# Kernel tuning notes

Hardware: AMD Instinct MI355X
Metric: run time of the kernel (lower is better)

Reference implementation:

```python
import jax, jax.numpy as jnp
import numpy as np

T, B, I, H, L = 512, 64, 512, 1024, 2

def setup_inputs() -> dict:
    key = jax.random.key(0)
    ks = jax.random.split(key, 9)
    stdv = 1.0 / np.sqrt(H)
    u = lambda k, shape: jax.random.uniform(k, shape, jnp.float32, -stdv, stdv)
    return {
        "x": jax.random.normal(ks[0], (T, B, I), jnp.float32),
        "w_ih0": u(ks[1], (4 * H, I)),
        "w_hh0": u(ks[2], (4 * H, H)),
        "b_ih0": u(ks[3], (4 * H,)),
        "b_hh0": u(ks[4], (4 * H,)),
        "w_ih1": u(ks[5], (4 * H, H)),
        "w_hh1": u(ks[6], (4 * H, H)),
        "b_ih1": u(ks[7], (4 * H,)),
        "b_hh1": u(ks[8], (4 * H,)),
    }

def _lstm_cell(x, h, c, w_ih, w_hh, b_ih, b_hh):
    # gates: [B, 4H]
    gates = x @ w_ih.T + b_ih + h @ w_hh.T + b_hh
    i, f, g, o = jnp.split(gates, 4, axis=1)
    c_new = jax.nn.sigmoid(f) * c + jax.nn.sigmoid(i) * jnp.tanh(g)
    h_new = jax.nn.sigmoid(o) * jnp.tanh(c_new)
    return h_new, c_new

def reference(x, w_ih0, w_hh0, b_ih0, b_hh0, w_ih1, w_hh1, b_ih1, b_hh1):
    layers = [(w_ih0, w_hh0, b_ih0, b_hh0), (w_ih1, w_hh1, b_ih1, b_hh1)]
    h0 = jnp.zeros((L, B, H), x.dtype)
    c0 = jnp.zeros((L, B, H), x.dtype)

    def step(carry, x_t):
        h, c = carry
        inp = x_t
        hs, cs = [], []
        for l, (w_ih, w_hh, b_ih, b_hh) in enumerate(layers):
            h_new, c_new = _lstm_cell(inp, h[l], c[l], w_ih, w_hh, b_ih, b_hh)
            hs.append(h_new)
            cs.append(c_new)
            inp = h_new
        return (jnp.stack(hs), jnp.stack(cs)), inp

    (h_f, c_f), out = jax.lax.scan(step, (h0, c0), x)
    return out, (h_f, c_f)
```

## Files before the change

kernel.cpp:

```cpp
#include <hip/hip_runtime.h>

#define TT 512
#define BB 64
#define II 512
#define HH 1024
#define NBLK 256
#define NTHR 512
#define FSTRIDE 32
#define SETSTRIDE (64 * FSTRIDE)

typedef short bf16x8 __attribute__((ext_vector_type(8)));
typedef float f32x4 __attribute__((ext_vector_type(4)));
typedef int   i32x4 __attribute__((ext_vector_type(4)));

struct Params {
  const unsigned short* xb;
  unsigned short* h0;
  unsigned short* h1;
  unsigned int* flags;
  const float* wih0; const float* whh0; const float* bih0; const float* bhh0;
  const float* wih1; const float* whh1; const float* bih1; const float* bhh1;
  float* out;
};

__device__ __forceinline__ unsigned short f2bf(float f) {
  unsigned int u = __float_as_uint(f);
  u += 0x7fffu + ((u >> 16) & 1u);
  return (unsigned short)(u >> 16);
}

__device__ __forceinline__ bf16x8 ld_bypass(const unsigned short* p) {
  i32x4 r;
  asm volatile("global_load_dwordx4 %0, %1, off sc0 sc1" : "=v"(r) : "v"(p));
  return __builtin_bit_cast(bf16x8, r);
}
__device__ __forceinline__ void st_bypass_b128(unsigned short* p, i32x4 v) {
  asm volatile("global_store_dwordx4 %0, %1, off sc0 sc1" :: "v"(p), "v"(v) : "memory");
}
__device__ __forceinline__ void st_bypass_u32(unsigned int* p, unsigned int v) {
  asm volatile("global_store_dword %0, %1, off sc0 sc1" :: "v"(p), "v"(v) : "memory");
}
__device__ __forceinline__ unsigned int ld_flag_bypass(const unsigned int* p) {
  unsigned int r;
  asm volatile("global_load_dword %0, %1, off sc0 sc1\n\t"
               "s_waitcnt vmcnt(0)" : "=v"(r) : "v"(p) : "memory");
  return r;
}

template <int SLP>
__device__ __forceinline__ void poll_set(const unsigned int* f, int lane,
                                         unsigned int tgt) {
  while (ld_flag_bypass(&f[lane * FSTRIDE]) < tgt)
    __builtin_amdgcn_s_sleep(SLP);
}

__global__ void cvt_kernel(const float* __restrict__ x, unsigned short* __restrict__ xb, int n8) {
  int i = blockIdx.x * blockDim.x + threadIdx.x;
  int stride = gridDim.x * blockDim.x;
  for (; i < n8; i += stride) {
    const float4* p = (const float4*)(x) + (size_t)i * 2;
    float4 a = p[0], b = p[1];
    bf16x8 v;
    v[0] = (short)f2bf(a.x); v[1] = (short)f2bf(a.y); v[2] = (short)f2bf(a.z); v[3] = (short)f2bf(a.w);
    v[4] = (short)f2bf(b.x); v[5] = (short)f2bf(b.y); v[6] = (short)f2bf(b.z); v[7] = (short)f2bf(b.w);
    ((bf16x8*)xb)[i] = v;
  }
}

template <int LAYER>
__device__ void body(const Params& P, float (*pbuf)[64][36], float (*cb)[16],
                     unsigned short (*hbuf)[16]) {
  constexpr int K   = (LAYER == 0) ? (II + HH) : (2 * HH);
  constexpr int KSL = K / (8 * 32);
  constexpr int NG  = KSL / 2;
  constexpr int KIH = (LAYER == 0) ? II : HH;

  const int tid  = threadIdx.x;
  const int lane = tid & 63;
  const int kh   = tid >> 6;
  const int lbid = blockIdx.x & 127;
  const int mh   = lbid >> 6;
  const int ns   = lbid & 63;
  const int l15  = lane & 15;
  const int lk8  = (lane >> 4) * 8;

  const int setL0 = mh;
  const int setL1 = 2 + mh;
  const int fset  = LAYER * 2 + mh;

  const float* wih = (LAYER == 0) ? P.wih0 : P.wih1;
  const float* whh = (LAYER == 0) ? P.whh0 : P.whh1;

  bf16x8 wf[4][KSL];
  #pragma unroll
  for (int nt = 0; nt < 4; ++nt) {
    const int row = nt * HH + ns * 16 + l15;
    #pragma unroll
    for (int ks = 0; ks < KSL; ++ks) {
      int k = kh * (KSL * 32) + ks * 32 + lk8;
      const float* src = (k < KIH) ? (wih + (size_t)row * KIH + k)
                                   : (whh + (size_t)row * HH + (k - KIH));
      const float4* p4 = (const float4*)src;
      float4 a = p4[0], b = p4[1];
      bf16x8 v;
      v[0] = (short)f2bf(a.x); v[1] = (short)f2bf(a.y); v[2] = (short)f2bf(a.z); v[3] = (short)f2bf(a.w);
      v[4] = (short)f2bf(b.x); v[5] = (short)f2bf(b.y); v[6] = (short)f2bf(b.z); v[7] = (short)f2bf(b.w);
      wf[nt][ks] = v;
    }
  }

  float bv[4];
  {
    const float* bi = (LAYER == 0) ? P.bih0 : P.bih1;
    const float* bh = (LAYER == 0) ? P.bhh0 : P.bhh1;
    int unit = ns * 16 + (tid & 15);
    #pragma unroll
    for (int g = 0; g < 4; ++g) bv[g] = bi[g * HH + unit] + bh[g * HH + unit];
  }

  if (tid < 128) {
    int q = tid >> 4, j = tid & 15;
    #pragma unroll
    for (int r = 0; r < 4; ++r) cb[q * 4 + r][j] = 0.f;
  }

  const size_t BH  = (size_t)BB * HH;
  const size_t TBH = (size_t)TT * BH;

  #pragma unroll 1
  for (int p = 0; p <= TT; ++p) {
    const int t = (LAYER == 0) ? p : p - 1;
    const bool active = (LAYER == 0) ? (p < TT) : (p >= 1);

    if (kh == 0 && p >= 1) {
      poll_set<1>(P.flags + (size_t)setL0 * SETSTRIDE, lane, (unsigned)p);
    }
    if (kh == 1) {
      if (LAYER == 0) {
        if (p >= 3) poll_set<8>(P.flags + (size_t)setL1 * SETSTRIDE, lane, (unsigned)(p - 2));
      } else {
        if (p >= 1) poll_set<1>(P.flags + (size_t)setL1 * SETSTRIDE, lane, (unsigned)p);
      }
    }
    __syncthreads();

    f32x4 acc[2][4];
    float hv[4];
    if (active) {
      #pragma unroll
      for (int mt = 0; mt < 2; ++mt)
        #pragma unroll
        for (int nt = 0; nt < 4; ++nt) acc[mt][nt] = f32x4{0.f, 0.f, 0.f, 0.f};

      const unsigned short* h0prev = P.h0 + (size_t)((t - 1) & 3) * BH;
      const unsigned short* h0cur  = P.h0 + (size_t)(t & 3) * BH;
      const unsigned short* h1prev = P.h1 + (size_t)((t - 1) & 3) * BH;

      bf16x8 af[2][2][2];

      auto issue_group = [&](int g, int pp) {
        #pragma unroll
        for (int ksb = 0; ksb < 2; ++ksb) {
          const int ks = g * 2 + ksb;
          const int k  = kh * (KSL * 32) + ks * 32 + lk8;
          #pragma unroll
          for (int mt = 0; mt < 2; ++mt) {
            const int m = mh * 32 + mt * 16 + l15;
            const unsigned short* src;
            if (LAYER == 0) {
              src = (k < II) ? (P.xb + ((size_t)t * BB + m) * II + k)
                             : (h0prev + (size_t)m * HH + (k - II));
            } else {
              src = (k < HH) ? (h0cur + (size_t)m * HH + k)
                             : (h1prev + (size_t)m * HH + (k - HH));
            }
            af[pp][ksb][mt] = ld_bypass(src);
          }
        }
      };

      issue_group(0, 0);
      issue_group(1, 1);
      #pragma unroll
      for (int g = 0; g < NG; ++g) {
        if (g < NG - 1) asm volatile("s_waitcnt vmcnt(4)" ::: "memory");
        else            asm volatile("s_waitcnt vmcnt(0)" ::: "memory");
        __builtin_amdgcn_sched_barrier(0);
        #pragma unroll
        for (int ksb = 0; ksb < 2; ++ksb) {
          const int ks = g * 2 + ksb;
          #pragma unroll
          for (int mt = 0; mt < 2; ++mt)
            #pragma unroll
            for (int nt = 0; nt < 4; ++nt)
              acc[mt][nt] = __builtin_amdgcn_mfma_f32_16x16x32_bf16(af[g & 1][ksb][mt], wf[nt][ks], acc[mt][nt], 0, 0, 0);
        }
        if (g + 2 < NG) issue_group(g + 2, g & 1);
      }

      if (kh >= 4) {
        #pragma unroll
        for (int mt = 0; mt < 2; ++mt)
          #pragma unroll
          for (int nt = 0; nt < 4; ++nt) {
            int col = nt * 16 + l15;
            int mb  = mt * 16 + (lane >> 4) * 4;
            *(f32x4*)&pbuf[kh - 4][col][mb] = acc[mt][nt];
          }
      }
    }
    __syncthreads();
    if (active && kh < 4) {
      #pragma unroll
      for (int mt = 0; mt < 2; ++mt)
        #pragma unroll
        for (int nt = 0; nt < 4; ++nt) {
          int col = nt * 16 + l15;
          int mb  = mt * 16 + (lane >> 4) * 4;
          f32x4 v = *(const f32x4*)&pbuf[kh][col][mb];
          acc[mt][nt] += v;
          *(f32x4*)&pbuf[kh][col][mb] = acc[mt][nt];
        }
    }
    __syncthreads();
    if (active && tid < 128) {
      int q = tid >> 4, j = tid & 15;
      f32x4 gv[4];
      #pragma unroll
      for (int g = 0; g < 4; ++g) {
        int col = g * 16 + j;
        f32x4 s = *(const f32x4*)&pbuf[0][col][q * 4];
        #pragma unroll
        for (int w = 1; w < 4; ++w) s += *(const f32x4*)&pbuf[w][col][q * 4];
        gv[g] = s;
      }
      #pragma unroll
      for (int r = 0; r < 4; ++r) {
        int m = q * 4 + r;
        float iv = 1.f / (1.f + __expf(-(gv[0][r] + bv[0])));
        float fv = 1.f / (1.f + __expf(-(gv[1][r] + bv[1])));
        float gg = tanhf(gv[2][r] + bv[2]);
        float ov = 1.f / (1.f + __expf(-(gv[3][r] + bv[3])));
        float c = fv * cb[m][j] + iv * gg;
        cb[m][j] = c;
        float h = ov * tanhf(c);
        hv[r] = h;
        hbuf[m][j] = f2bf(h);
      }
    }
    __syncthreads();
    if (tid < 64) {
      if (active) {
        int row  = tid >> 1;
        int half = tid & 1;
        i32x4 v = *(const i32x4*)&hbuf[row][half * 8];
        unsigned short* dst = ((LAYER == 0) ? P.h0 : P.h1) +
            (size_t)(t & 3) * BH + (size_t)(mh * 32 + row) * HH + ns * 16 + half * 8;
        st_bypass_b128(dst, v);
      }
      asm volatile("s_waitcnt vmcnt(0)" ::: "memory");
      if (tid == 0)
        st_bypass_u32(P.flags + (size_t)fset * SETSTRIDE + (size_t)ns * FSTRIDE,
                      (unsigned)(p + 1));
    }
    if (active && tid < 128) {
      int q = tid >> 4, j = tid & 15;
      #pragma unroll
      for (int r = 0; r < 4; ++r) {
        int mg = mh * 32 + q * 4 + r;
        int unit = ns * 16 + j;
        if (LAYER == 0) {
          if (t == TT - 1) P.out[TBH + (size_t)mg * HH + unit] = hv[r];
        } else {
          P.out[(size_t)t * BH + (size_t)mg * HH + unit] = hv[r];
          if (t == TT - 1) P.out[TBH + BH + (size_t)mg * HH + unit] = hv[r];
        }
      }
    }
  }

  if (tid < 128) {
    int q = tid >> 4, j = tid & 15;
    #pragma unroll
    for (int r = 0; r < 4; ++r) {
      int m = q * 4 + r;
      int mg = mh * 32 + m;
      int unit = ns * 16 + j;
      P.out[TBH + (size_t)(2 + LAYER) * BH + (size_t)mg * HH + unit] = cb[m][j];
    }
  }
}

__global__ void __launch_bounds__(NTHR, 1) lstm_kernel(Params P) {
  __shared__ float pbuf[4][64][36];
  __shared__ float cb[32][16];
  __shared__ unsigned short hbuf[32][16];
  if (blockIdx.x < 128) body<0>(P, pbuf, cb, hbuf);
  else                  body<1>(P, pbuf, cb, hbuf);
}

extern "C" void kernel_launch(void* const* d_in, const int* in_sizes, int n_in,
                              void* d_out, int out_size, void* d_ws, size_t ws_size,
                              hipStream_t stream) {
  const float* x = (const float*)d_in[0];
  Params P;
  P.wih0 = (const float*)d_in[1];
  P.whh0 = (const float*)d_in[2];
  P.bih0 = (const float*)d_in[3];
  P.bhh0 = (const float*)d_in[4];
  P.wih1 = (const float*)d_in[5];
  P.whh1 = (const float*)d_in[6];
  P.bih1 = (const float*)d_in[7];
  P.bhh1 = (const float*)d_in[8];
  P.out  = (float*)d_out;

  char* ws = (char*)d_ws;
  P.flags = (unsigned int*)ws;
  P.xb  = (const unsigned short*)(ws + 32768);
  unsigned short* xb_w = (unsigned short*)(ws + 32768);
  P.h0  = (unsigned short*)(ws + 32768 + (size_t)TT * BB * II * 2);
  P.h1  = P.h0 + (size_t)4 * BB * HH;

  (void)hipMemsetAsync((void*)P.flags, 0, 32768, stream);
  (void)hipMemsetAsync((void*)P.h0, 0, (size_t)8 * BB * HH * sizeof(unsigned short), stream);

  int n8 = TT * BB * II / 8;
  cvt_kernel<<<2048, 256, 0, stream>>>(x, xb_w, n8);

  void* args[] = { &P };
  (void)hipLaunchCooperativeKernel((void*)lstm_kernel, dim3(NBLK), dim3(NTHR), args, 0, stream);
}
```

Before: 3.844 ms.

## Give each wave a fixed 256-wide K slice and per-wave flag polling

New measurement: 4.842 ms. +26.0%, slower.

```diff
diff --git a/kernel.cpp b/kernel.cpp
--- a/kernel.cpp
+++ b/kernel.cpp
@@ -68,11 +68,10 @@
 }
 
 template <int LAYER>
-__device__ void body(const Params& P, float (*pbuf)[64][36], float (*cb)[16],
+__device__ void body(const Params& P, float (*pbuf)[64][40], float (*cb)[16],
                      unsigned short (*hbuf)[16]) {
-  constexpr int K   = (LAYER == 0) ? (II + HH) : (2 * HH);
-  constexpr int KSL = K / (8 * 32);
-  constexpr int NG  = KSL / 2;
+  constexpr int NW  = (LAYER == 0) ? 6 : 8;
+  constexpr int KSL = 8;
   constexpr int KIH = (LAYER == 0) ? II : HH;
 
   const int tid  = threadIdx.x;
@@ -92,20 +91,22 @@
   const float* whh = (LAYER == 0) ? P.whh0 : P.whh1;
 
   bf16x8 wf[4][KSL];
-  #pragma unroll
-  for (int nt = 0; nt < 4; ++nt) {
-    const int row = nt * HH + ns * 16 + l15;
+  if (kh < NW) {
     #pragma unroll
-    for (int ks = 0; ks < KSL; ++ks) {
-      int k = kh * (KSL * 32) + ks * 32 + lk8;
-      const float* src = (k < KIH) ? (wih + (size_t)row * KIH + k)
-                                   : (whh + (size_t)row * HH + (k - KIH));
-      const float4* p4 = (const float4*)src;
-      float4 a = p4[0], b = p4[1];
-      bf16x8 v;
-      v[0] = (short)f2bf(a.x); v[1] = (short)f2bf(a.y); v[2] = (short)f2bf(a.z); v[3] = (short)f2bf(a.w);
-      v[4] = (short)f2bf(b.x); v[5] = (short)f2bf(b.y); v[6] = (short)f2bf(b.z); v[7] = (short)f2bf(b.w);
-      wf[nt][ks] = v;
+    for (int nt = 0; nt < 4; ++nt) {
+      const int row = nt * HH + ns * 16 + l15;
+      #pragma unroll
+      for (int ks = 0; ks < KSL; ++ks) {
+        int k = kh * 256 + ks * 32 + lk8;
+        const float* src = (k < KIH) ? (wih + (size_t)row * KIH + k)
+                                     : (whh + (size_t)row * HH + (k - KIH));
+        const float4* p4 = (const float4*)src;
+        float4 a = p4[0], b = p4[1];
+        bf16x8 v;
+        v[0] = (short)f2bf(a.x); v[1] = (short)f2bf(a.y); v[2] = (short)f2bf(a.z); v[3] = (short)f2bf(a.w);
+        v[4] = (short)f2bf(b.x); v[5] = (short)f2bf(b.y); v[6] = (short)f2bf(b.z); v[7] = (short)f2bf(b.w);
+        wf[nt][ks] = v;
+      }
     }
   }
 
@@ -132,21 +133,16 @@
     const int t = (LAYER == 0) ? p : p - 1;
     const bool active = (LAYER == 0) ? (p < TT) : (p >= 1);
 
-    if (kh == 0 && p >= 1) {
-      poll_set<1>(P.flags + (size_t)setL0 * SETSTRIDE, lane, (unsigned)p);
-    }
-    if (kh == 1) {
-      if (LAYER == 0) {
-        if (p >= 3) poll_set<8>(P.flags + (size_t)setL1 * SETSTRIDE, lane, (unsigned)(p - 2));
-      } else {
-        if (p >= 1) poll_set<1>(P.flags + (size_t)setL1 * SETSTRIDE, lane, (unsigned)p);
-      }
-    }
-    __syncthreads();
-
     f32x4 acc[2][4];
     float hv[4];
-    if (active) {
+    if (active && kh < NW) {
+      if (LAYER == 0) {
+        if (kh >= 2) poll_set<1>(P.flags + (size_t)setL0 * SETSTRIDE, lane, (unsigned)p);
+      } else {
+        if (kh < 4)  poll_set<1>(P.flags + (size_t)setL0 * SETSTRIDE, lane, (unsigned)p);
+        else         poll_set<1>(P.flags + (size_t)setL1 * SETSTRIDE, lane, (unsigned)p);
+      }
+
       #pragma unroll
       for (int mt = 0; mt < 2; ++mt)
         #pragma unroll
@@ -156,13 +152,13 @@
       const unsigned short* h0cur  = P.h0 + (size_t)(t & 3) * BH;
       const unsigned short* h1prev = P.h1 + (size_t)((t - 1) & 3) * BH;
 
-      bf16x8 af[2][2][2];
-
-      auto issue_group = [&](int g, int pp) {
+      bf16x8 af[3][2][2];
+
+      auto issue_group = [&](int g, int slot) {
         #pragma unroll
         for (int ksb = 0; ksb < 2; ++ksb) {
           const int ks = g * 2 + ksb;
-          const int k  = kh * (KSL * 32) + ks * 32 + lk8;
+          const int k  = kh * 256 + ks * 32 + lk8;
           #pragma unroll
           for (int mt = 0; mt < 2; ++mt) {
             const int m = mh * 32 + mt * 16 + l15;
@@ -174,18 +170,21 @@
               src = (k < HH) ? (h0cur + (size_t)m * HH + k)
                              : (h1prev + (size_t)m * HH + (k - HH));
             }
-            af[pp][ksb][mt] = ld_bypass(src);
+            af[slot][ksb][mt] = ld_bypass(src);
           }
         }
       };
 
       issue_group(0, 0);
       issue_group(1, 1);
-      #pragma unroll
-      for (int g = 0; g < NG; ++g) {
-        if (g < NG - 1) asm volatile("s_waitcnt vmcnt(4)" ::: "memory");
-        else            asm volatile("s_waitcnt vmcnt(0)" ::: "memory");
+      issue_group(2, 2);
+      #pragma unroll
+      for (int g = 0; g < 4; ++g) {
+        if (g < 2)       asm volatile("s_waitcnt vmcnt(8)" ::: "memory");
+        else if (g == 2) asm volatile("s_waitcnt vmcnt(4)" ::: "memory");
+        else             asm volatile("s_waitcnt vmcnt(0)" ::: "memory");
         __builtin_amdgcn_sched_barrier(0);
+        const int slot = (g == 3) ? 0 : g;
         #pragma unroll
         for (int ksb = 0; ksb < 2; ++ksb) {
           const int ks = g * 2 + ksb;
@@ -193,36 +192,25 @@
           for (int mt = 0; mt < 2; ++mt)
             #pragma unroll
             for (int nt = 0; nt < 4; ++nt)
-              acc[mt][nt] = __builtin_amdgcn_mfma_f32_16x16x32_bf16(af[g & 1][ksb][mt], wf[nt][ks], acc[mt][nt], 0, 0, 0);
+              acc[mt][nt] = __builtin_amdgcn_mfma_f32_16x16x32_bf16(af[slot][ksb][mt], wf[nt][ks], acc[mt][nt], 0, 0, 0);
         }
-        if (g + 2 < NG) issue_group(g + 2, g & 1);
-      }
-
-      if (kh >= 4) {
-        #pragma unroll
-        for (int mt = 0; mt < 2; ++mt)
-          #pragma unroll
-          for (int nt = 0; nt < 4; ++nt) {
-            int col = nt * 16 + l15;
-            int mb  = mt * 16 + (lane >> 4) * 4;
-            *(f32x4*)&pbuf[kh - 4][col][mb] = acc[mt][nt];
-          }
-      }
-    }
-    __syncthreads();
-    if (active && kh < 4) {
+        if (g == 0) issue_group(3, 0);
+      }
+
       #pragma unroll
       for (int mt = 0; mt < 2; ++mt)
         #pragma unroll
         for (int nt = 0; nt < 4; ++nt) {
           int col = nt * 16 + l15;
           int mb  = mt * 16 + (lane >> 4) * 4;
-          f32x4 v = *(const f32x4*)&pbuf[kh][col][mb];
-          acc[mt][nt] += v;
           *(f32x4*)&pbuf[kh][col][mb] = acc[mt][nt];
         }
     }
+    if (LAYER == 0 && active && kh == 6 && p >= 3)
+      poll_set<8>(P.flags + (size_t)setL1 * SETSTRIDE, lane, (unsigned)(p - 2));
+
     __syncthreads();
+
     if (active && tid < 128) {
       int q = tid >> 4, j = tid & 15;
       f32x4 gv[4];
@@ -231,7 +219,7 @@
         int col = g * 16 + j;
         f32x4 s = *(const f32x4*)&pbuf[0][col][q * 4];
         #pragma unroll
-        for (int w = 1; w < 4; ++w) s += *(const f32x4*)&pbuf[w][col][q * 4];
+        for (int w = 1; w < NW; ++w) s += *(const f32x4*)&pbuf[w][col][q * 4];
         gv[g] = s;
       }
       #pragma unroll
@@ -249,6 +237,7 @@
       }
     }
     __syncthreads();
+
     if (tid < 64) {
       if (active) {
         int row  = tid >> 1;
@@ -277,6 +266,7 @@
         }
       }
     }
+    asm volatile("s_waitcnt vmcnt(0)" ::: "memory");
   }
 
   if (tid < 128) {
@@ -292,7 +282,7 @@
 }
 
 __global__ void __launch_bounds__(NTHR, 1) lstm_kernel(Params P) {
-  __shared__ float pbuf[4][64][36];
+  __shared__ float pbuf[8][64][40];
   __shared__ float cb[32][16];
   __shared__ unsigned short hbuf[32][16];
   if (blockIdx.x < 128) body<0>(P, pbuf, cb, hbuf);
```

## Pack sync flags densely and poll them with vectorized loads

Applied to the files above, without the earlier changes.

Measured after the change: 4.914 ms. 27.8% more time.

```diff
diff --git a/kernel.cpp b/kernel.cpp
--- a/kernel.cpp
+++ b/kernel.cpp
@@ -6,8 +6,7 @@
 #define HH 1024
 #define NBLK 256
 #define NTHR 512
-#define FSTRIDE 32
-#define SETSTRIDE (64 * FSTRIDE)
+#define SETSTRIDE 128
 
 typedef short bf16x8 __attribute__((ext_vector_type(8)));
 typedef float f32x4 __attribute__((ext_vector_type(4)));
@@ -40,18 +39,20 @@
 __device__ __forceinline__ void st_bypass_u32(unsigned int* p, unsigned int v) {
   asm volatile("global_store_dword %0, %1, off sc0 sc1" :: "v"(p), "v"(v) : "memory");
 }
-__device__ __forceinline__ unsigned int ld_flag_bypass(const unsigned int* p) {
-  unsigned int r;
-  asm volatile("global_load_dword %0, %1, off sc0 sc1\n\t"
-               "s_waitcnt vmcnt(0)" : "=v"(r) : "v"(p) : "memory");
-  return r;
-}
 
 template <int SLP>
 __device__ __forceinline__ void poll_set(const unsigned int* f, int lane,
                                          unsigned int tgt) {
-  while (ld_flag_bypass(&f[lane * FSTRIDE]) < tgt)
+  const unsigned int* addr = f + (lane & 15) * 4;
+  for (;;) {
+    i32x4 v;
+    asm volatile("global_load_dwordx4 %0, %1, off sc0 sc1\n\t"
+                 "s_waitcnt vmcnt(0)" : "=v"(v) : "v"(addr) : "memory");
+    bool ok = ((unsigned)v[0] >= tgt) && ((unsigned)v[1] >= tgt) &&
+              ((unsigned)v[2] >= tgt) && ((unsigned)v[3] >= tgt);
+    if (__all(ok)) break;
     __builtin_amdgcn_s_sleep(SLP);
+  }
 }
 
 __global__ void cvt_kernel(const float* __restrict__ x, unsigned short* __restrict__ xb, int n8) {
@@ -133,13 +134,13 @@
     const bool active = (LAYER == 0) ? (p < TT) : (p >= 1);
 
     if (kh == 0 && p >= 1) {
-      poll_set<1>(P.flags + (size_t)setL0 * SETSTRIDE, lane, (unsigned)p);
+      poll_set<2>(P.flags + (size_t)setL0 * SETSTRIDE, lane, (unsigned)p);
     }
     if (kh == 1) {
       if (LAYER == 0) {
         if (p >= 3) poll_set<8>(P.flags + (size_t)setL1 * SETSTRIDE, lane, (unsigned)(p - 2));
       } else {
-        if (p >= 1) poll_set<1>(P.flags + (size_t)setL1 * SETSTRIDE, lane, (unsigned)p);
+        if (p >= 1) poll_set<2>(P.flags + (size_t)setL1 * SETSTRIDE, lane, (unsigned)p);
       }
     }
     __syncthreads();
@@ -166,15 +167,13 @@
           #pragma unroll
           for (int mt = 0; mt < 2; ++mt) {
             const int m = mh * 32 + mt * 16 + l15;
-            const unsigned short* src;
             if (LAYER == 0) {
-              src = (k < II) ? (P.xb + ((size_t)t * BB + m) * II + k)
-                             : (h0prev + (size_t)m * HH + (k - II));
+              if (k < II) af[pp][ksb][mt] = *(const bf16x8*)(P.xb + ((size_t)t * BB + m) * II + k);
+              else        af[pp][ksb][mt] = ld_bypass(h0prev + (size_t)m * HH + (k - II));
             } else {
-              src = (k < HH) ? (h0cur + (size_t)m * HH + k)
-                             : (h1prev + (size_t)m * HH + (k - HH));
+              if (k < HH) af[pp][ksb][mt] = ld_bypass(h0cur + (size_t)m * HH + k);
+              else        af[pp][ksb][mt] = ld_bypass(h1prev + (size_t)m * HH + (k - HH));
             }
-            af[pp][ksb][mt] = ld_bypass(src);
           }
         }
       };
@@ -260,8 +259,7 @@
       }
       asm volatile("s_waitcnt vmcnt(0)" ::: "memory");
       if (tid == 0)
-        st_bypass_u32(P.flags + (size_t)fset * SETSTRIDE + (size_t)ns * FSTRIDE,
-                      (unsigned)(p + 1));
+        st_bypass_u32(P.flags + (size_t)fset * SETSTRIDE + ns, (unsigned)(p + 1));
     }
     if (active && tid < 128) {
       int q = tid >> 4, j = tid & 15;
```
